# Kernel tuning notes

Hardware: AMD Instinct MI355X
Metric: run time of the kernel (lower is better)

Reference implementation:

```python
import jax, jax.numpy as jnp
import numpy as np

EMB = 768
HEADS = 12
HEAD_DIM = EMB // HEADS  # 64
SCALE = HEAD_DIM ** -0.5


def setup_inputs() -> dict:
    key = jax.random.key(0)
    ks = jax.random.split(key, 9)
    B, S = 32, 576
    s = EMB ** -0.5
    return {
        "hidden_states": jax.random.normal(ks[0], (B, S, EMB), jnp.float32),
        "q_w": jax.random.normal(ks[1], (EMB, EMB), jnp.float32) * s,
        "q_b": jnp.zeros((EMB,), jnp.float32),
        "k_w": jax.random.normal(ks[2], (EMB, EMB), jnp.float32) * s,
        "k_b": jnp.zeros((EMB,), jnp.float32),
        "v_w": jax.random.normal(ks[3], (EMB, EMB), jnp.float32) * s,
        "v_b": jnp.zeros((EMB,), jnp.float32),
        "o_w": jax.random.normal(ks[4], (EMB, EMB), jnp.float32) * s,
        "o_b": jnp.zeros((EMB,), jnp.float32),
    }


def reference(hidden_states, q_w, q_b, k_w, k_b, v_w, v_b, o_w, o_b):
    B, S, _ = hidden_states.shape
    # Linear projections (torch Linear: x @ W^T + b)
    q = hidden_states @ q_w.T + q_b
    k = hidden_states @ k_w.T + k_b
    v = hidden_states @ v_w.T + v_b
    # [B, H, S, D]
    q = q.reshape(B, S, HEADS, HEAD_DIM).transpose(0, 2, 1, 3)
    k = k.reshape(B, S, HEADS, HEAD_DIM).transpose(0, 2, 1, 3)
    v = v.reshape(B, S, HEADS, HEAD_DIM).transpose(0, 2, 1, 3)
    # Full N x N attention scores, softmax in fp32 (as in source)
    scores = jnp.einsum('bhqd,bhkd->bhqk', q, k) * SCALE
    attn = jax.nn.softmax(scores.astype(jnp.float32), axis=-1).astype(q.dtype)
    # dropout p=0.0 -> identity
    out = jnp.einsum('bhqk,bhkd->bhqd', attn, v)  # [B, H, S, D]
    out = out.transpose(0, 2, 1, 3).reshape(B, S, EMB)
    out = out @ o_w.T + o_b
    return (out, attn)
```

## Files before the change

### kernel.cpp

```cpp
#include <hip/hip_runtime.h>


#define B_ 32
#define S_ 576
#define H_ 12
#define D_ 64
#define E_ 768
#define M_ (B_ * S_)

typedef __attribute__((ext_vector_type(8))) short bf16x8;
typedef __attribute__((ext_vector_type(4))) float f32x4;
typedef __attribute__((ext_vector_type(4))) unsigned short u16x4;
typedef __attribute__((ext_vector_type(8))) unsigned short u16x8;

#define MFMA16(a, b, c) __builtin_amdgcn_mfma_f32_16x16x32_bf16(a, b, c, 0, 0, 0)

__device__ __forceinline__ unsigned short f2bf(float x) {
  union { float f; unsigned u; } v; v.f = x;
  unsigned r = v.u + 0x7fffu + ((v.u >> 16) & 1u);
  return (unsigned short)(r >> 16);
}
__device__ __forceinline__ float bf2f(unsigned short h) {
  union { unsigned u; float f; } v; v.u = ((unsigned)h) << 16; return v.f;
}

__global__ __launch_bounds__(256) void cvt_split(const float* __restrict__ in,
                                                 unsigned short* __restrict__ hi,
                                                 unsigned short* __restrict__ lo,
                                                 int n4) {
  int i = blockIdx.x * 256 + threadIdx.x;
  if (i >= n4) return;
  float4 x = ((const float4*)in)[i];
  u16x4 h;
  h[0] = f2bf(x.x); h[1] = f2bf(x.y); h[2] = f2bf(x.z); h[3] = f2bf(x.w);
  ((u16x4*)hi)[i] = h;
  if (lo) {
    u16x4 l;
    l[0] = f2bf(x.x - bf2f(h[0])); l[1] = f2bf(x.y - bf2f(h[1]));
    l[2] = f2bf(x.z - bf2f(h[2])); l[3] = f2bf(x.w - bf2f(h[3]));
    ((u16x4*)lo)[i] = l;
  }
}

template <bool SPLIT, int OUT_MODE>
__global__ __launch_bounds__(256)
void gemm128(const unsigned short* __restrict__ Ahg, const unsigned short* __restrict__ Alg,
             const unsigned short* __restrict__ Bhg, const unsigned short* __restrict__ Blg,
             const float* __restrict__ bias, void* __restrict__ C0, void* __restrict__ C1,
             int Kd, int lda, int ldb, int ldc) {
  constexpr int BM = 128, BN = 128, BK = 32, LSTR = BK + 8;
  __shared__ __attribute__((aligned(16))) unsigned short Ah[BM * LSTR];
  __shared__ __attribute__((aligned(16))) unsigned short Bh[BN * LSTR];
  __shared__ __attribute__((aligned(16))) unsigned short Al[SPLIT ? BM * LSTR : 8];
  __shared__ __attribute__((aligned(16))) unsigned short Bl[SPLIT ? BN * LSTR : 8];

  const int tid = threadIdx.x, lane = tid & 63, wv = tid >> 6;
  const int wm = (wv & 1) * 64, wn = (wv >> 1) * 64;
  const long m0 = (long)blockIdx.y * BM, n0 = (long)blockIdx.x * BN;
  const int fr = lane & 15, g8 = (lane >> 4) * 8;

  f32x4 acc[4][4] = {};

  for (int kt = 0; kt < Kd; kt += BK) {
    __syncthreads();
    for (int i = tid; i < BM * BK / 8; i += 256) {
      int row = i >> 2, c8 = (i & 3) * 8;
      *(u16x8*)&Ah[row * LSTR + c8] = *(const u16x8*)(Ahg + (m0 + row) * lda + kt + c8);
      *(u16x8*)&Bh[row * LSTR + c8] = *(const u16x8*)(Bhg + (n0 + row) * ldb + kt + c8);
      if (SPLIT) {
        *(u16x8*)&Al[row * LSTR + c8] = *(const u16x8*)(Alg + (m0 + row) * lda + kt + c8);
        *(u16x8*)&Bl[row * LSTR + c8] = *(const u16x8*)(Blg + (n0 + row) * ldb + kt + c8);
      }
    }
    __syncthreads();
    bf16x8 ah[4], bh[4], al[4], bl[4];
#pragma unroll
    for (int mi = 0; mi < 4; ++mi) {
      ah[mi] = *(const bf16x8*)&Ah[(wm + mi * 16 + fr) * LSTR + g8];
      if (SPLIT) al[mi] = *(const bf16x8*)&Al[(wm + mi * 16 + fr) * LSTR + g8];
    }
#pragma unroll
    for (int ni = 0; ni < 4; ++ni) {
      bh[ni] = *(const bf16x8*)&Bh[(wn + ni * 16 + fr) * LSTR + g8];
      if (SPLIT) bl[ni] = *(const bf16x8*)&Bl[(wn + ni * 16 + fr) * LSTR + g8];
    }
#pragma unroll
    for (int mi = 0; mi < 4; ++mi)
#pragma unroll
      for (int ni = 0; ni < 4; ++ni) {
        acc[mi][ni] = MFMA16(ah[mi], bh[ni], acc[mi][ni]);
        if (SPLIT) {
          acc[mi][ni] = MFMA16(ah[mi], bl[ni], acc[mi][ni]);
          acc[mi][ni] = MFMA16(al[mi], bh[ni], acc[mi][ni]);
        }
      }
  }

#pragma unroll
  for (int mi = 0; mi < 4; ++mi)
#pragma unroll
    for (int ni = 0; ni < 4; ++ni) {
      long col = n0 + wn + ni * 16 + fr;
      long rb = m0 + wm + mi * 16 + (lane >> 4) * 4;
      float bv = bias ? bias[col] : 0.f;
#pragma unroll
      for (int r = 0; r < 4; ++r) {
        float v = acc[mi][ni][r] + bv;
        long idx = (rb + r) * ldc + col;
        if (OUT_MODE == 0) {
          ((float*)C0)[idx] = v;
        } else if (OUT_MODE == 1) {
          ((unsigned short*)C0)[idx] = f2bf(v);
        } else if (OUT_MODE == 2) {
          unsigned short hh = f2bf(v);
          ((unsigned short*)C0)[idx] = hh;
          ((unsigned short*)C1)[idx] = f2bf(v - bf2f(hh));
        } else {
          long m = rb + r;
          int bb = (int)(m / S_);
          int ss = (int)(m - (long)bb * S_);
          int hh2 = (int)(col >> 6), dd = (int)(col & 63);
          ((unsigned short*)C0)[(((long)bb * H_ + hh2) * D_ + dd) * S_ + ss] = f2bf(v);
        }
      }
    }
}

__global__ __launch_bounds__(256)
void attn_pv(const unsigned short* __restrict__ qh, const unsigned short* __restrict__ ql,
             const unsigned short* __restrict__ kh, const unsigned short* __restrict__ kl,
             const unsigned short* __restrict__ vt,
             float* __restrict__ attn, unsigned short* __restrict__ out_pre) {
  constexpr int LQ = 72;
  constexpr int LP = 584;
  __shared__ __attribute__((aligned(16))) unsigned short qhl[32 * LQ], qll[32 * LQ];
  __shared__ __attribute__((aligned(16))) unsigned short khl[64 * LQ], kll[64 * LQ];
  __shared__ __attribute__((aligned(16))) unsigned short P_lds[32 * LP];
  __shared__ float redm[2][32], reds[2][32];
  unsigned short* Vt = kll;

  const int tid = threadIdx.x, lane = tid & 63, wv = tid >> 6;
  const int qt = blockIdx.x, h = blockIdx.y, b = blockIdx.z;
  const int fr = lane & 15, gq = lane >> 4;
  const int mg = (wv & 1), ch = (wv >> 1);

  {
    int row = tid >> 3, c8 = (tid & 7) * 8;
    long qb = ((long)(b * S_ + qt * 32 + row)) * E_ + h * 64 + c8;
    *(u16x8*)&qhl[row * LQ + c8] = *(const u16x8*)(qh + qb);
    *(u16x8*)&qll[row * LQ + c8] = *(const u16x8*)(ql + qb);
  }
  __syncthreads();
  bf16x8 qa_h[2], qa_l[2];
#pragma unroll
  for (int kc = 0; kc < 2; ++kc) {
    qa_h[kc] = *(const bf16x8*)&qhl[(mg * 16 + fr) * LQ + kc * 32 + gq * 8];
    qa_l[kc] = *(const bf16x8*)&qll[(mg * 16 + fr) * LQ + kc * 32 + gq * 8];
  }

  f32x4 acc[9][2] = {};
  for (int kt = 0; kt < 9; ++kt) {
    __syncthreads();
    for (int i = tid; i < 512; i += 256) {
      int row = i >> 3, c8 = (i & 7) * 8;
      long kb = ((long)(b * S_ + kt * 64 + row)) * E_ + h * 64 + c8;
      *(u16x8*)&khl[row * LQ + c8] = *(const u16x8*)(kh + kb);
      *(u16x8*)&kll[row * LQ + c8] = *(const u16x8*)(kl + kb);
    }
    __syncthreads();
#pragma unroll
    for (int kc = 0; kc < 2; ++kc) {
#pragma unroll
      for (int nf = 0; nf < 2; ++nf) {
        bf16x8 b_h = *(const bf16x8*)&khl[(ch * 32 + nf * 16 + fr) * LQ + kc * 32 + gq * 8];
        bf16x8 b_l = *(const bf16x8*)&kll[(ch * 32 + nf * 16 + fr) * LQ + kc * 32 + gq * 8];
        acc[kt][nf] = MFMA16(qa_h[kc], b_h, acc[kt][nf]);
        acc[kt][nf] = MFMA16(qa_h[kc], b_l, acc[kt][nf]);
        acc[kt][nf] = MFMA16(qa_l[kc], b_h, acc[kt][nf]);
      }
    }
  }

  const float SC = 0.125f;
  float M[4], Sv[4];
#pragma unroll
  for (int r = 0; r < 4; ++r) {
    float pm = -1e30f;
#pragma unroll
    for (int kt = 0; kt < 9; ++kt)
#pragma unroll
      for (int nf = 0; nf < 2; ++nf) pm = fmaxf(pm, acc[kt][nf][r] * SC);
    for (int off = 1; off < 16; off <<= 1) pm = fmaxf(pm, __shfl_xor(pm, off));
    M[r] = pm;
  }
  if (fr == 0) {
#pragma unroll
    for (int r = 0; r < 4; ++r) redm[ch][mg * 16 + gq * 4 + r] = M[r];
  }
  __syncthreads();
#pragma unroll
  for (int r = 0; r < 4; ++r)
    M[r] = fmaxf(redm[0][mg * 16 + gq * 4 + r], redm[1][mg * 16 + gq * 4 + r]);

#pragma unroll
  for (int r = 0; r < 4; ++r) {
    float ps = 0.f;
#pragma unroll
    for (int kt = 0; kt < 9; ++kt)
#pragma unroll
      for (int nf = 0; nf < 2; ++nf) {
        float e = __expf(acc[kt][nf][r] * SC - M[r]);
        acc[kt][nf][r] = e;
        ps += e;
      }
    for (int off = 1; off < 16; off <<= 1) ps += __shfl_xor(ps, off);
    Sv[r] = ps;
  }
  if (fr == 0) {
#pragma unroll
    for (int r = 0; r < 4; ++r) reds[ch][mg * 16 + gq * 4 + r] = Sv[r];
  }
  __syncthreads();
#pragma unroll
  for (int r = 0; r < 4; ++r)
    Sv[r] = 1.f / (reds[0][mg * 16 + gq * 4 + r] + reds[1][mg * 16 + gq * 4 + r]);

  float* out = attn + ((long)((b * H_ + h) * S_) + qt * 32) * S_;
#pragma unroll
  for (int kt = 0; kt < 9; ++kt)
#pragma unroll
    for (int nf = 0; nf < 2; ++nf)
#pragma unroll
      for (int r = 0; r < 4; ++r) {
        int row = mg * 16 + gq * 4 + r;
        int col = kt * 64 + ch * 32 + nf * 16 + fr;
        float val = acc[kt][nf][r] * Sv[r];
        __builtin_nontemporal_store(val, &out[(long)row * S_ + col]);
        P_lds[row * LP + col] = f2bf(val);
      }

  const unsigned short* Vb = vt + ((long)(b * H_ + h)) * D_ * S_;
  f32x4 accp[2] = {};
  for (int kt2 = 0; kt2 < 9; ++kt2) {
    __syncthreads();
    for (int i = tid; i < 512; i += 256) {
      int row = i >> 3, c8 = (i & 7) * 8;
      *(u16x8*)&Vt[row * LQ + c8] = *(const u16x8*)(Vb + (long)row * S_ + kt2 * 64 + c8);
    }
    __syncthreads();
#pragma unroll
    for (int kc = 0; kc < 2; ++kc) {
      bf16x8 a = *(const bf16x8*)&P_lds[(mg * 16 + fr) * LP + kt2 * 64 + kc * 32 + gq * 8];
#pragma unroll
      for (int ni = 0; ni < 2; ++ni) {
        bf16x8 bv = *(const bf16x8*)&Vt[(ch * 32 + ni * 16 + fr) * LQ + kc * 32 + gq * 8];
        accp[ni] = MFMA16(a, bv, accp[ni]);
      }
    }
  }

#pragma unroll
  for (int ni = 0; ni < 2; ++ni)
#pragma unroll
    for (int r = 0; r < 4; ++r) {
      int row = mg * 16 + gq * 4 + r;
      int col = ch * 32 + ni * 16 + fr;
      out_pre[((long)b * S_ + qt * 32 + row) * E_ + h * 64 + col] = f2bf(accp[ni][r]);
    }
}

extern "C" void kernel_launch(void* const* d_in, const int* in_sizes, int n_in,
                              void* d_out, int out_size, void* d_ws, size_t ws_size,
                              hipStream_t stream) {
  const float* X = (const float*)d_in[0];
  const float* q_w = (const float*)d_in[1];
  const float* q_b = (const float*)d_in[2];
  const float* k_w = (const float*)d_in[3];
  const float* k_b = (const float*)d_in[4];
  const float* v_w = (const float*)d_in[5];
  const float* v_b = (const float*)d_in[6];
  const float* o_w = (const float*)d_in[7];
  const float* o_b = (const float*)d_in[8];

  const long NX = (long)M_ * E_;
  const long NW = (long)E_ * E_;

  unsigned short* w = (unsigned short*)d_ws;
  unsigned short* Xhi = w;
  unsigned short* Xlo = Xhi + NX;
  unsigned short* qwh = Xlo + NX;
  unsigned short* qwl = qwh + NW;
  unsigned short* kwh = qwl + NW;
  unsigned short* kwl = kwh + NW;
  unsigned short* vwh = kwl + NW;
  unsigned short* owh = vwh + NW;
  unsigned short* Qhi = owh + NW;
  unsigned short* Qlo = Qhi + NX;
  unsigned short* Khi = Qlo + NX;
  unsigned short* Klo = Khi + NX;
  unsigned short* Vt  = Klo + NX;
  unsigned short* Opre = Vt + NX;

  float* out_f = (float*)d_out;
  float* attn_f = (float*)d_out + NX;

  cvt_split<<<dim3((NX / 4 + 255) / 256), dim3(256), 0, stream>>>(X, Xhi, Xlo, NX / 4);
  cvt_split<<<dim3((NW / 4 + 255) / 256), dim3(256), 0, stream>>>(q_w, qwh, qwl, NW / 4);
  cvt_split<<<dim3((NW / 4 + 255) / 256), dim3(256), 0, stream>>>(k_w, kwh, kwl, NW / 4);
  cvt_split<<<dim3((NW / 4 + 255) / 256), dim3(256), 0, stream>>>(v_w, vwh, nullptr, NW / 4);
  cvt_split<<<dim3((NW / 4 + 255) / 256), dim3(256), 0, stream>>>(o_w, owh, nullptr, NW / 4);

  dim3 gproj(E_ / 128, M_ / 128);
  gemm128<true, 2><<<gproj, dim3(256), 0, stream>>>(Xhi, Xlo, qwh, qwl, q_b, Qhi, Qlo, E_, E_, E_, E_);
  gemm128<true, 2><<<gproj, dim3(256), 0, stream>>>(Xhi, Xlo, kwh, kwl, k_b, Khi, Klo, E_, E_, E_, E_);
  gemm128<false, 3><<<gproj, dim3(256), 0, stream>>>(Xhi, nullptr, vwh, nullptr, v_b, Vt, nullptr, E_, E_, E_, E_);

  attn_pv<<<dim3(S_ / 32, H_, B_), dim3(256), 0, stream>>>(Qhi, Qlo, Khi, Klo, Vt, attn_f, Opre);

  gemm128<false, 0><<<gproj, dim3(256), 0, stream>>>(Opre, nullptr, owh, nullptr, o_b, out_f, nullptr, E_, E_, E_, E_);
}
```

Before: 1.197 ms.

## Load GEMM tiles directly into LDS and alias attention shared buffers

The GEMM tile loads now use global_load_lds direct-to-LDS transfers, which means an unpadded LDS layout (stride BK instead of BK+8). That removes the register round trip but may add LDS bank conflicts on the fragment reads. The attention kernel folds its separate shared arrays into one buffer where P overlaps Q/K, cutting LDS footprint so more blocks can be resident. The nontemporal store for the attention-probability output is replaced with a normal store. Aliasing P over Q/K depends on Q and K no longer being needed when P is written.

```diff
diff --git a/kernel.cpp b/kernel.cpp
--- a/kernel.cpp
+++ b/kernel.cpp
@@ -22,6 +22,12 @@
 }
 __device__ __forceinline__ float bf2f(unsigned short h) {
   union { unsigned u; float f; } v; v.u = ((unsigned)h) << 16; return v.f;
+}
+
+__device__ __forceinline__ void gload16(unsigned short* lds, const unsigned short* g) {
+  __builtin_amdgcn_global_load_lds(
+      (const __attribute__((address_space(1))) unsigned int*)g,
+      (__attribute__((address_space(3))) unsigned int*)lds, 16, 0, 0);
 }
 
 __global__ __launch_bounds__(256) void cvt_split(const float* __restrict__ in,
@@ -48,41 +54,46 @@
              const unsigned short* __restrict__ Bhg, const unsigned short* __restrict__ Blg,
              const float* __restrict__ bias, void* __restrict__ C0, void* __restrict__ C1,
              int Kd, int lda, int ldb, int ldc) {
-  constexpr int BM = 128, BN = 128, BK = 32, LSTR = BK + 8;
-  __shared__ __attribute__((aligned(16))) unsigned short Ah[BM * LSTR];
-  __shared__ __attribute__((aligned(16))) unsigned short Bh[BN * LSTR];
-  __shared__ __attribute__((aligned(16))) unsigned short Al[SPLIT ? BM * LSTR : 8];
-  __shared__ __attribute__((aligned(16))) unsigned short Bl[SPLIT ? BN * LSTR : 8];
+  constexpr int BM = 128, BN = 128, BK = 32;
+  __shared__ __attribute__((aligned(16))) unsigned short Ah[BM * BK];
+  __shared__ __attribute__((aligned(16))) unsigned short Bh[BN * BK];
+  __shared__ __attribute__((aligned(16))) unsigned short Al[SPLIT ? BM * BK : 8];
+  __shared__ __attribute__((aligned(16))) unsigned short Bl[SPLIT ? BN * BK : 8];
 
   const int tid = threadIdx.x, lane = tid & 63, wv = tid >> 6;
   const int wm = (wv & 1) * 64, wn = (wv >> 1) * 64;
   const long m0 = (long)blockIdx.y * BM, n0 = (long)blockIdx.x * BN;
   const int fr = lane & 15, g8 = (lane >> 4) * 8;
+  const int srow = lane >> 2, sc8 = (lane & 3) * 8;
 
   f32x4 acc[4][4] = {};
 
   for (int kt = 0; kt < Kd; kt += BK) {
     __syncthreads();
-    for (int i = tid; i < BM * BK / 8; i += 256) {
-      int row = i >> 2, c8 = (i & 3) * 8;
-      *(u16x8*)&Ah[row * LSTR + c8] = *(const u16x8*)(Ahg + (m0 + row) * lda + kt + c8);
-      *(u16x8*)&Bh[row * LSTR + c8] = *(const u16x8*)(Bhg + (n0 + row) * ldb + kt + c8);
+#pragma unroll
+    for (int c = 0; c < 2; ++c) {
+      int chunk = wv * 2 + c;
+      int row = chunk * 16 + srow;
+      long ga = (m0 + row) * (long)lda + kt + sc8;
+      long gb = (n0 + row) * (long)ldb + kt + sc8;
+      gload16(&Ah[chunk * 512], Ahg + ga);
+      gload16(&Bh[chunk * 512], Bhg + gb);
       if (SPLIT) {
-        *(u16x8*)&Al[row * LSTR + c8] = *(const u16x8*)(Alg + (m0 + row) * lda + kt + c8);
-        *(u16x8*)&Bl[row * LSTR + c8] = *(const u16x8*)(Blg + (n0 + row) * ldb + kt + c8);
+        gload16(&Al[chunk * 512], Alg + ga);
+        gload16(&Bl[chunk * 512], Blg + gb);
       }
     }
     __syncthreads();
     bf16x8 ah[4], bh[4], al[4], bl[4];
 #pragma unroll
     for (int mi = 0; mi < 4; ++mi) {
-      ah[mi] = *(const bf16x8*)&Ah[(wm + mi * 16 + fr) * LSTR + g8];
-      if (SPLIT) al[mi] = *(const bf16x8*)&Al[(wm + mi * 16 + fr) * LSTR + g8];
+      ah[mi] = *(const bf16x8*)&Ah[(wm + mi * 16 + fr) * BK + g8];
+      if (SPLIT) al[mi] = *(const bf16x8*)&Al[(wm + mi * 16 + fr) * BK + g8];
     }
 #pragma unroll
     for (int ni = 0; ni < 4; ++ni) {
-      bh[ni] = *(const bf16x8*)&Bh[(wn + ni * 16 + fr) * LSTR + g8];
-      if (SPLIT) bl[ni] = *(const bf16x8*)&Bl[(wn + ni * 16 + fr) * LSTR + g8];
+      bh[ni] = *(const bf16x8*)&Bh[(wn + ni * 16 + fr) * BK + g8];
+      if (SPLIT) bl[ni] = *(const bf16x8*)&Bl[(wn + ni * 16 + fr) * BK + g8];
     }
 #pragma unroll
     for (int mi = 0; mi < 4; ++mi)
@@ -133,10 +144,13 @@
              float* __restrict__ attn, unsigned short* __restrict__ out_pre) {
   constexpr int LQ = 72;
   constexpr int LP = 584;
-  __shared__ __attribute__((aligned(16))) unsigned short qhl[32 * LQ], qll[32 * LQ];
-  __shared__ __attribute__((aligned(16))) unsigned short khl[64 * LQ], kll[64 * LQ];
-  __shared__ __attribute__((aligned(16))) unsigned short P_lds[32 * LP];
+  __shared__ __attribute__((aligned(16))) unsigned short smem[23296];
   __shared__ float redm[2][32], reds[2][32];
+  unsigned short* qhl = smem;
+  unsigned short* qll = smem + 2304;
+  unsigned short* khl = smem + 4608;
+  unsigned short* kll = smem + 18688;
+  unsigned short* P_lds = smem;
   unsigned short* Vt = kll;
 
   const int tid = threadIdx.x, lane = tid & 63, wv = tid >> 6;
@@ -235,7 +249,7 @@
         int row = mg * 16 + gq * 4 + r;
         int col = kt * 64 + ch * 32 + nf * 16 + fr;
         float val = acc[kt][nf][r] * Sv[r];
-        __builtin_nontemporal_store(val, &out[(long)row * S_ + col]);
+        out[(long)row * S_ + col] = val;
         P_lds[row * LP + col] = f2bf(val);
       }
 
```

New measurement: 1.163 ms. 1.03x faster.
